# Kernel tuning notes

Measured on AMD Instinct MI355X. Metric: run time of the kernel, lower is better.

## Reference

```python
import jax, jax.numpy as jnp
import numpy as np

B, S, D, H = 16, 512, 1024, 16
DK = D // H
DFF = 4 * D
EPS = 1e-5
NEG = -1e9


def fake_quant(w):
    # EMA int8 symmetric per-tensor fake quantization of weights (inference view)
    scale = jnp.max(jnp.abs(w)) / 127.0
    wq = jnp.round(w / scale) * scale
    # straight-through estimator form (no-op in fwd)
    return w + jax.lax.stop_gradient(wq - w)


def layer_norm(x, g, b):
    mu = jnp.mean(x, axis=-1, keepdims=True)
    var = jnp.mean(jnp.square(x - mu), axis=-1, keepdims=True)
    return (x - mu) * jax.lax.rsqrt(var + EPS) * g + b


def setup_inputs() -> dict:
    key = jax.random.key(0)
    ks = jax.random.split(key, 16)
    std = 0.02
    inp = {
        'x': jax.random.normal(ks[0], (B, S, D), jnp.float32),
        'mask': jax.random.randint(ks[1], (B, 1, S, S), 0, 2, jnp.int32),
        'wq': jax.random.normal(ks[2], (D, D), jnp.float32) * std,
        'bq': jnp.zeros((D,), jnp.float32),
        'wk': jax.random.normal(ks[3], (D, D), jnp.float32) * std,
        'bk': jnp.zeros((D,), jnp.float32),
        'wv': jax.random.normal(ks[4], (D, D), jnp.float32) * std,
        'bv': jnp.zeros((D,), jnp.float32),
        'wo': jax.random.normal(ks[5], (D, D), jnp.float32) * std,
        'bo': jnp.zeros((D,), jnp.float32),
        'w1': jax.random.normal(ks[6], (D, DFF), jnp.float32) * std,
        'b1': jnp.zeros((DFF,), jnp.float32),
        'w2': jax.random.normal(ks[7], (DFF, D), jnp.float32) * std,
        'b2': jnp.zeros((D,), jnp.float32),
        'ln1_g': jnp.ones((D,), jnp.float32),
        'ln1_b': jnp.zeros((D,), jnp.float32),
        'ln2_g': jnp.ones((D,), jnp.float32),
        'ln2_b': jnp.zeros((D,), jnp.float32),
        'layer': 0,
    }
    return inp


def reference(x, mask, wq, bq, wk, bk, wv, bv, wo, bo, w1, b1, w2, b2,
              ln1_g, ln1_b, ln2_g, ln2_b, layer):
    # --- input sublayer: x + attention(LN(x)) (dropout = identity at eval) ---
    h = layer_norm(x, ln1_g, ln1_b)
    q = (h @ fake_quant(wq) + bq).reshape(B, S, H, DK).transpose(0, 2, 1, 3)
    k = (h @ fake_quant(wk) + bk).reshape(B, S, H, DK).transpose(0, 2, 1, 3)
    v = (h @ fake_quant(wv) + bv).reshape(B, S, H, DK).transpose(0, 2, 1, 3)
    scores = jnp.einsum('bhqd,bhkd->bhqk', q, k) * (1.0 / np.sqrt(DK))
    scores = jnp.where(mask == 0, NEG, scores)
    p = jax.nn.softmax(scores, axis=-1)
    attn = jnp.einsum('bhqk,bhkd->bhqd', p, v)
    attn = attn.transpose(0, 2, 1, 3).reshape(B, S, D)
    x = x + (attn @ wo + bo)
    # --- output sublayer: x + FFN(LN(x)), gelu (exact), middle_drop=False ---
    h2 = layer_norm(x, ln2_g, ln2_b)
    ff = jax.nn.gelu(h2 @ w1 + b1, approximate=False) @ w2 + b2
    return x + ff
```

## Files before the change

kernel.cpp:

```cpp
#include <hip/hip_runtime.h>
#include <hip/hip_bf16.h>
#include <math.h>

#define B_   16
#define S_   512
#define D_   1024
#define H_   16
#define DK_  64
#define DFF_ 4096
#define NROW (B_ * S_)
#define NEG_ (-1.0e9f)
#define SCQ_ 0.18033688011112042f

typedef __attribute__((ext_vector_type(8))) short short8v;
typedef __attribute__((ext_vector_type(4))) float f32x4;

__device__ __forceinline__ void load_lds16(const void* g, void* l) {
    __builtin_amdgcn_global_load_lds(
        reinterpret_cast<const __attribute__((address_space(1))) unsigned int*>(
            reinterpret_cast<uintptr_t>(g)),
        reinterpret_cast<__attribute__((address_space(3))) unsigned int*>(
            reinterpret_cast<uintptr_t>(l)),
        16, 0, 0);
}

__device__ __forceinline__ ushort f2bf_raw(float f) {
    __hip_bfloat16 h = __float2bfloat16(f);
    return *(ushort*)&h;
}

__device__ __forceinline__ float gelu_f(float v) {
    return 0.5f * v * (1.0f + erff(v * 0.70710678118654752f));
}

__global__ __launch_bounds__(256) void maskpack_k(
    const int* __restrict__ mask, unsigned long long* __restrict__ bits,
    unsigned int* __restrict__ scales) {
    if (blockIdx.x == 0 && threadIdx.x < 3) scales[threadIdx.x] = 0u;
    const int g = blockIdx.x * 4 + (threadIdx.x >> 6);
    const unsigned long long bm = __ballot(mask[(size_t)g * 64 + (threadIdx.x & 63)] != 0);
    if ((threadIdx.x & 63) == 0) bits[g] = bm;
}

__global__ __launch_bounds__(256) void maxabs3_k(
    const float* __restrict__ wq, const float* __restrict__ wk,
    const float* __restrict__ wv, unsigned int* __restrict__ out, int n) {
    const int wi = blockIdx.y;
    const float* w = wi == 0 ? wq : (wi == 1 ? wk : wv);
    float m = 0.f;
    for (int i = blockIdx.x * blockDim.x + threadIdx.x; i < n; i += gridDim.x * blockDim.x)
        m = fmaxf(m, fabsf(w[i]));
#pragma unroll
    for (int off = 1; off < 64; off <<= 1)
        m = fmaxf(m, __shfl_xor(m, off));
    __shared__ float red[4];
    const int wave = threadIdx.x >> 6;
    if ((threadIdx.x & 63) == 0) red[wave] = m;
    __syncthreads();
    if (threadIdx.x == 0) {
        m = fmaxf(fmaxf(red[0], red[1]), fmaxf(red[2], red[3]));
        atomicMax(out + wi, __float_as_uint(m));
    }
}

__global__ __launch_bounds__(256) void transq_all_k(
    const float* __restrict__ wq, const float* __restrict__ wk,
    const float* __restrict__ wv, const float* __restrict__ wo,
    const float* __restrict__ w1, const float* __restrict__ w2,
    const unsigned int* __restrict__ scales,
    __hip_bfloat16* __restrict__ wcat,
    __hip_bfloat16* __restrict__ wot,
    __hip_bfloat16* __restrict__ w1t, __hip_bfloat16* __restrict__ w2t)
{
    const int bid = blockIdx.x;
    int wi, rem, nbn, K, N;
    if (bid < 4096)      { wi = bid >> 10; rem = bid & 1023; nbn = 32;  K = 1024; N = 1024; }
    else if (bid < 8192) { wi = 4; rem = bid - 4096;         nbn = 128; K = 1024; N = 4096; }
    else                 { wi = 5; rem = bid - 8192;         nbn = 32;  K = 4096; N = 1024; }
    const float* W = wi == 0 ? wq : wi == 1 ? wk : wi == 2 ? wv : wi == 3 ? wo : wi == 4 ? w1 : w2;
    __hip_bfloat16* Wt = wi < 3 ? wcat + (size_t)wi * 1024 * 1024
                       : wi == 3 ? wot : wi == 4 ? w1t : w2t;
    const int n0 = (rem % nbn) * 32, k0 = (rem / nbn) * 32;

    __shared__ float t[32][33];
    const int tx = threadIdx.x, ty = threadIdx.y;
    float scale = 1.0f;
    const bool doq = wi < 3;
    if (doq) scale = __uint_as_float(scales[wi]) * (1.0f / 127.0f);
#pragma unroll
    for (int i = 0; i < 4; ++i) {
        float v = W[(size_t)(k0 + ty + 8 * i) * N + n0 + tx];
        if (doq) v = rintf(v / scale) * scale;
        t[ty + 8 * i][tx] = v;
    }
    __syncthreads();
#pragma unroll
    for (int i = 0; i < 4; ++i)
        Wt[(size_t)(n0 + ty + 8 * i) * K + k0 + tx] = __float2bfloat16(t[tx][ty + 8 * i]);
}

__global__ __launch_bounds__(256) void ln_bf16_k(
    const float* __restrict__ x, const float* __restrict__ g,
    const float* __restrict__ b, __hip_bfloat16* __restrict__ y)
{
    const int row = blockIdx.x;
    const int tid = threadIdx.x;
    const float4 v = *(const float4*)&x[(size_t)row * D_ + tid * 4];

    float s = v.x + v.y + v.z + v.w;
#pragma unroll
    for (int off = 1; off < 64; off <<= 1) s += __shfl_xor(s, off);
    __shared__ float red[8];
    const int wave = tid >> 6, lane = tid & 63;
    if (lane == 0) red[wave] = s;
    __syncthreads();
    s = red[0] + red[1] + red[2] + red[3];
    const float mu = s * (1.0f / (float)D_);

    const float d0 = v.x - mu, d1 = v.y - mu, d2 = v.z - mu, d3 = v.w - mu;
    float sq = d0 * d0 + d1 * d1 + d2 * d2 + d3 * d3;
#pragma unroll
    for (int off = 1; off < 64; off <<= 1) sq += __shfl_xor(sq, off);
    if (lane == 0) red[4 + wave] = sq;
    __syncthreads();
    sq = red[4] + red[5] + red[6] + red[7];
    const float rs = 1.0f / sqrtf(sq * (1.0f / (float)D_) + 1e-5f);

    const float4 gv = *(const float4*)&g[tid * 4];
    const float4 bv = *(const float4*)&b[tid * 4];
    union { ushort4 u4; ushort u[4]; } cv;
    cv.u[0] = f2bf_raw(d0 * rs * gv.x + bv.x);
    cv.u[1] = f2bf_raw(d1 * rs * gv.y + bv.y);
    cv.u[2] = f2bf_raw(d2 * rs * gv.z + bv.z);
    cv.u[3] = f2bf_raw(d3 * rs * gv.w + bv.w);
    *(ushort4*)&y[(size_t)row * D_ + tid * 4] = cv.u4;
}

template <int BNT, int EPI>
__global__ __launch_bounds__(512, 2) void gemm256(
    const __hip_bfloat16* __restrict__ A, const __hip_bfloat16* __restrict__ Bt,
    const float* __restrict__ bias, const float* __restrict__ bias2,
    const float* __restrict__ bias3, const float* __restrict__ res,
    void* __restrict__ C, void* __restrict__ C2, void* __restrict__ C3,
    int M, int N, int K)
{
    constexpr int BN   = BNT * 64;
    constexpr int ABYT = 256 * 128;
    constexpr int BBYT = BN * 128;
    constexpr int BUF  = ABYT + BBYT;
    constexpr int SB   = BNT / 2;
    __shared__ __align__(16) char smem[2 * BUF];

    const int tid = threadIdx.x;
    const int w = tid >> 6, lane = tid & 63;
    const int llo = lane & 15, lhi = lane >> 4;
    const int wr = w >> 2, wc = w & 3;

    const int nwg = gridDim.x;
    const int bid = blockIdx.x;
    const int swz = (bid & 7) * (nwg >> 3) + (bid >> 3);
    const int nby = M >> 8;
    const int by = swz % nby, bx = swz / nby;
    const int row0 = by * 256, col0 = bx * BN;

    const int cko0 = ((lhi) ^ (llo & 7)) * 16;
    const int cko1 = ((4 + lhi) ^ (llo & 7)) * 16;

    const int l3 = lane >> 3;
    const int klog8 = ((lane & 7) ^ l3) * 8;
    const int rA_base = ((w >> 1) & 3) * 16 + (w & 1) * 8 + l3;
    const int rB_ws = w * 8 + l3;

    const __hip_bfloat16* Asrc[2][2];
#pragma unroll
    for (int h = 0; h < 2; ++h)
#pragma unroll
        for (int s = 0; s < 2; ++s)
            Asrc[h][s] = A + (size_t)(row0 + s * 128 + h * 64 + rA_base) * K + klog8;
    const __hip_bfloat16* Bsrc[2][2];
#pragma unroll
    for (int h = 0; h < 2; ++h)
#pragma unroll
        for (int s = 0; s < 2; ++s)
            Bsrc[h][s] = Bt + (size_t)(col0 + h * (BN / 2) + (SB == 2 ? s * 64 : 0) + rB_ws) * K + klog8;

#define STAGE_A(bufv, hh, tt) do {                                                            \
    load_lds16(Asrc[hh][0] + (size_t)(tt) * 64, smem + (bufv) * BUF + (hh) * 16384 + w * 1024);        \
    load_lds16(Asrc[hh][1] + (size_t)(tt) * 64, smem + (bufv) * BUF + (hh) * 16384 + 8192 + w * 1024); \
} while (0)
#define STAGE_B(bufv, hh, tt) do {                                                                     \
    load_lds16(Bsrc[hh][0] + (size_t)(tt) * 64, smem + (bufv) * BUF + ABYT + (hh) * (BBYT / 2) + w * 1024); \
    if (SB == 2)                                                                                       \
        load_lds16(Bsrc[hh][1] + (size_t)(tt) * 64, smem + (bufv) * BUF + ABYT + (hh) * (BBYT / 2) + 8192 + w * 1024); \
} while (0)

    f32x4 acc[8][BNT] = {};
    const int NT = K >> 6;

    STAGE_B(0, 0, 0); STAGE_B(0, 1, 0); STAGE_A(0, 0, 0); STAGE_A(0, 1, 0);
    asm volatile("s_waitcnt vmcnt(0)");
    __builtin_amdgcn_s_barrier();

    short8v bfr[BNT][2];
    for (int t = 0; t < NT; ++t) {
        const int buf = t & 1;
        const bool more = (t + 1) < NT;
        char* const base = smem + buf * BUF;
#pragma unroll
        for (int ph = 0; ph < 4; ++ph) {
            if (ph == 0) {
#pragma unroll
                for (int n = 0; n < BNT; ++n) {
                    const int brow = wc * (BNT * 16) + n * 16 + llo;
                    bfr[n][0] = *(const short8v*)(base + ABYT + brow * 128 + cko0);
                    bfr[n][1] = *(const short8v*)(base + ABYT + brow * 128 + cko1);
                }
            }
            const int mf0 = ph * 2, mf1 = ph * 2 + 1;
            const int slot0 = (mf0 >> 2) * 128 + wr * 64 + (mf0 & 3) * 16 + llo;
            const int slot1 = (mf1 >> 2) * 128 + wr * 64 + (mf1 & 3) * 16 + llo;
            const short8v a0k0 = *(const short8v*)(base + slot0 * 128 + cko0);
            const short8v a0k1 = *(const short8v*)(base + slot0 * 128 + cko1);
            const short8v a1k0 = *(const short8v*)(base + slot1 * 128 + cko0);
            const short8v a1k1 = *(const short8v*)(base + slot1 * 128 + cko1);
            if (more) {
                if (ph == 0) { STAGE_B(buf ^ 1, 0, t + 1); STAGE_B(buf ^ 1, 1, t + 1); }
                else if (ph == 1) { STAGE_A(buf ^ 1, 0, t + 1); STAGE_A(buf ^ 1, 1, t + 1); }
            }
            __builtin_amdgcn_s_barrier();
            __builtin_amdgcn_s_setprio(1);
#pragma unroll
            for (int n = 0; n < BNT; ++n) {
                acc[mf0][n] = __builtin_amdgcn_mfma_f32_16x16x32_bf16(a0k0, bfr[n][0], acc[mf0][n], 0, 0, 0);
                acc[mf0][n] = __builtin_amdgcn_mfma_f32_16x16x32_bf16(a0k1, bfr[n][1], acc[mf0][n], 0, 0, 0);
                acc[mf1][n] = __builtin_amdgcn_mfma_f32_16x16x32_bf16(a1k0, bfr[n][0], acc[mf1][n], 0, 0, 0);
                acc[mf1][n] = __builtin_amdgcn_mfma_f32_16x16x32_bf16(a1k1, bfr[n][1], acc[mf1][n], 0, 0, 0);
            }
            __builtin_amdgcn_s_setprio(0);
            if (ph == 3) { asm volatile("s_waitcnt vmcnt(0)"); }
            __builtin_amdgcn_s_barrier();
        }
    }
#undef STAGE_A
#undef STAGE_B

    if (EPI == 3) {
#pragma unroll
        for (int n = 0; n < BNT; ++n) {
            const int col = col0 + wc * (BNT * 16) + n * 16 + llo;
            const int proj = col0 >> 10;
            const int lcol = col & 1023;
            const float bs = (proj == 0 ? bias : proj == 1 ? bias2 : bias3)[lcol];
#pragma unroll
            for (int mf = 0; mf < 8; ++mf) {
                const int rbase = row0 + wr * 128 + mf * 16 + lhi * 4;
                if (proj == 2) {
                    const int bb = rbase >> 9, srow = rbase & 511;
                    const int hh = lcol >> 6, dk = lcol & 63;
                    union { ushort4 u4; ushort u[4]; } pk;
#pragma unroll
                    for (int j = 0; j < 4; ++j) pk.u[j] = f2bf_raw(acc[mf][n][j] + bs);
                    *(ushort4*)&((ushort*)C3)[(((size_t)(bb * 16 + hh) * 64 + dk) << 9) + srow] = pk.u4;
                } else {
                    __hip_bfloat16* dst = proj == 0 ? (__hip_bfloat16*)C : (__hip_bfloat16*)C2;
                    const float sc = proj == 0 ? SCQ_ : 1.0f;
#pragma unroll
                    for (int j = 0; j < 4; ++j)
                        dst[(size_t)(rbase + j) * D_ + lcol] = __float2bfloat16((acc[mf][n][j] + bs) * sc);
                }
            }
        }
    } else {
        constexpr int WCOL = BNT * 16;
        constexpr int ESTR = WCOL + 4;
        float* const eslab = (float*)smem + w * (16 * ESTR);
        const int rr = lane >> 2;
        const int cq = lane & 3;
        const int c0 = cq * (BNT * 4);
        const int gcolb = col0 + wc * WCOL + c0;
#pragma unroll
        for (int mf = 0; mf < 8; ++mf) {
#pragma unroll
            for (int n = 0; n < BNT; ++n)
#pragma unroll
                for (int j = 0; j < 4; ++j)
                    eslab[(lhi * 4 + j) * ESTR + n * 16 + llo] = acc[mf][n][j];
            const int grow = row0 + wr * 128 + mf * 16 + rr;
            if (EPI == 1) {
                ushort tmp[BNT * 4];
#pragma unroll
                for (int i = 0; i < BNT; ++i) {
                    float4 v = *(float4*)&eslab[rr * ESTR + c0 + i * 4];
                    const float4 b4 = *(const float4*)&bias[gcolb + i * 4];
                    tmp[i * 4 + 0] = f2bf_raw(gelu_f(v.x + b4.x));
                    tmp[i * 4 + 1] = f2bf_raw(gelu_f(v.y + b4.y));
                    tmp[i * 4 + 2] = f2bf_raw(gelu_f(v.z + b4.z));
                    tmp[i * 4 + 3] = f2bf_raw(gelu_f(v.w + b4.w));
                }
                ushort* dst = (ushort*)C + (size_t)grow * N + gcolb;
#pragma unroll
                for (int i = 0; i < BNT / 2; ++i)
                    *(short8v*)(dst + i * 8) = *(short8v*)&tmp[i * 8];
            } else {
#pragma unroll
                for (int i = 0; i < BNT; ++i) {
                    float4 v = *(float4*)&eslab[rr * ESTR + c0 + i * 4];
                    const float4 b4 = *(const float4*)&bias[gcolb + i * 4];
                    const float4 r4 = *(const float4*)&res[(size_t)grow * N + gcolb + i * 4];
                    v.x += b4.x + r4.x;
                    v.y += b4.y + r4.y;
                    v.z += b4.z + r4.z;
                    v.w += b4.w + r4.w;
                    *(float4*)&((float*)C)[(size_t)grow * N + gcolb + i * 4] = v;
                }
            }
        }
    }
}

__global__ __launch_bounds__(256) void attn_mfma_k(
    const __hip_bfloat16* __restrict__ q, const __hip_bfloat16* __restrict__ k,
    const __hip_bfloat16* __restrict__ vt, const unsigned long long* __restrict__ mbits,
    __hip_bfloat16* __restrict__ o)
{
    const int qt = blockIdx.x;
    const int bh = blockIdx.y;
    const int b = bh >> 4, h = bh & 15;

    __shared__ __align__(16) __hip_bfloat16 Qs[64 * 72];
    __shared__ __align__(16) __hip_bfloat16 Ks[64 * 72];
    __shared__ __align__(16) __hip_bfloat16 Vts[64 * 72];
    __shared__ __align__(16) __hip_bfloat16 Pt[64 * 72];

    const int tid = threadIdx.x;
    const int w = tid >> 6, l = tid & 63;
    const int llo = l & 15, lhi = l >> 4;
    const int srow = tid >> 2, schk = tid & 3;

    {
        const __hip_bfloat16* qg =
            q + (size_t)(b * S_ + qt * 64 + srow) * D_ + h * 64 + schk * 16;
        *(short8v*)&Qs[srow * 72 + schk * 16] = *(const short8v*)qg;
        *(short8v*)&Qs[srow * 72 + schk * 16 + 8] = *(const short8v*)(qg + 8);
    }

    const __hip_bfloat16* kptr = k + (size_t)(b * S_ + srow) * D_ + h * 64 + schk * 16;
    const __hip_bfloat16* vptr = vt + (((size_t)(b * 16 + h) * 64 + srow) << 9) + schk * 16;
    short8v kr0 = *(const short8v*)kptr;
    short8v kr1 = *(const short8v*)(kptr + 8);
    short8v vr0 = *(const short8v*)vptr;
    short8v vr1 = *(const short8v*)(vptr + 8);

    __syncthreads();

    const short8v qa0 = *(const short8v*)&Qs[(w * 16 + llo) * 72 + lhi * 8];
    const short8v qa1 = *(const short8v*)&Qs[(w * 16 + llo) * 72 + 32 + lhi * 8];

    const unsigned long long* mrow =
        mbits + (((size_t)(b * S_ + qt * 64 + w * 16 + lhi * 4)) << 3);

    f32x4 oacc[4] = {};
    float m_r[4] = {-INFINITY, -INFINITY, -INFINITY, -INFINITY};
    float l_r[4] = {0.f, 0.f, 0.f, 0.f};

    for (int kt = 0; kt < 8; ++kt) {
        *(short8v*)&Ks[srow * 72 + schk * 16] = kr0;
        *(short8v*)&Ks[srow * 72 + schk * 16 + 8] = kr1;
        *(short8v*)&Vts[srow * 72 + schk * 16] = vr0;
        *(short8v*)&Vts[srow * 72 + schk * 16 + 8] = vr1;
        __syncthreads();

        short8v nk0, nk1, nv0, nv1;
        if (kt < 7) {
            const __hip_bfloat16* kp = kptr + (size_t)(kt + 1) * (64 * D_);
            const __hip_bfloat16* vp = vptr + (kt + 1) * 64;
            nk0 = *(const short8v*)kp;
            nk1 = *(const short8v*)(kp + 8);
            nv0 = *(const short8v*)vp;
            nv1 = *(const short8v*)(vp + 8);
        }

        f32x4 sacc[4] = {};
#pragma unroll
        for (int n = 0; n < 4; ++n)
            sacc[n] = __builtin_amdgcn_mfma_f32_16x16x32_bf16(
                qa0, *(const short8v*)&Ks[(n * 16 + llo) * 72 + lhi * 8], sacc[n], 0, 0, 0);
#pragma unroll
        for (int n = 0; n < 4; ++n)
            sacc[n] = __builtin_amdgcn_mfma_f32_16x16x32_bf16(
                qa1, *(const short8v*)&Ks[(n * 16 + llo) * 72 + 32 + lhi * 8], sacc[n], 0, 0, 0);

#pragma unroll
        for (int j = 0; j < 4; ++j) {
            const unsigned long long mb = mrow[j * 8 + kt];
            const float s0 = ((mb >> llo) & 1ull)        ? sacc[0][j] : NEG_;
            const float s1 = ((mb >> (llo + 16)) & 1ull) ? sacc[1][j] : NEG_;
            const float s2 = ((mb >> (llo + 32)) & 1ull) ? sacc[2][j] : NEG_;
            const float s3 = ((mb >> (llo + 48)) & 1ull) ? sacc[3][j] : NEG_;
            float pm = fmaxf(fmaxf(s0, s1), fmaxf(s2, s3));
            pm = fmaxf(pm, __shfl_xor(pm, 1));
            pm = fmaxf(pm, __shfl_xor(pm, 2));
            pm = fmaxf(pm, __shfl_xor(pm, 4));
            pm = fmaxf(pm, __shfl_xor(pm, 8));
            float alpha = 1.0f;
            if (!__all(pm <= m_r[j] + 8.0f)) {
                const float mnew = fmaxf(m_r[j], pm);
                alpha = exp2f(m_r[j] - mnew);
                m_r[j] = mnew;
#pragma unroll
                for (int df = 0; df < 4; ++df) oacc[df][j] *= alpha;
            }
            const float p0 = exp2f(s0 - m_r[j]);
            const float p1 = exp2f(s1 - m_r[j]);
            const float p2 = exp2f(s2 - m_r[j]);
            const float p3 = exp2f(s3 - m_r[j]);
            float rsum = p0 + p1 + p2 + p3;
            rsum += __shfl_xor(rsum, 1);
            rsum += __shfl_xor(rsum, 2);
            rsum += __shfl_xor(rsum, 4);
            rsum += __shfl_xor(rsum, 8);
            l_r[j] = l_r[j] * alpha + rsum;
            const int prow = (w * 16 + lhi * 4 + j) * 72;
            Pt[prow + llo]      = __float2bfloat16(p0);
            Pt[prow + llo + 16] = __float2bfloat16(p1);
            Pt[prow + llo + 32] = __float2bfloat16(p2);
            Pt[prow + llo + 48] = __float2bfloat16(p3);
        }

#pragma unroll
        for (int ks = 0; ks < 2; ++ks) {
            const short8v pa = *(const short8v*)&Pt[(w * 16 + llo) * 72 + ks * 32 + lhi * 8];
#pragma unroll
            for (int df = 0; df < 4; ++df) {
                const short8v vb = *(const short8v*)&Vts[(df * 16 + llo) * 72 + ks * 32 + lhi * 8];
                oacc[df] = __builtin_amdgcn_mfma_f32_16x16x32_bf16(pa, vb, oacc[df], 0, 0, 0);
            }
        }
        __syncthreads();

        if (kt < 7) { kr0 = nk0; kr1 = nk1; vr0 = nv0; vr1 = nv1; }
    }

#pragma unroll
    for (int j = 0; j < 4; ++j) {
        const float inv = 1.0f / l_r[j];
        __hip_bfloat16* orow =
            o + (size_t)(b * S_ + qt * 64 + w * 16 + lhi * 4 + j) * D_ + h * 64;
#pragma unroll
        for (int df = 0; df < 4; ++df)
            orow[df * 16 + llo] = __float2bfloat16(oacc[df][j] * inv);
    }
}

extern "C" void kernel_launch(void* const* d_in, const int* in_sizes, int n_in,
                              void* d_out, int out_size, void* d_ws, size_t ws_size,
                              hipStream_t stream)
{
    const float* x    = (const float*)d_in[0];
    const int*   mask = (const int*)d_in[1];
    const float* wq   = (const float*)d_in[2];
    const float* bq   = (const float*)d_in[3];
    const float* wk   = (const float*)d_in[4];
    const float* bk   = (const float*)d_in[5];
    const float* wv   = (const float*)d_in[6];
    const float* bv   = (const float*)d_in[7];
    const float* wo   = (const float*)d_in[8];
    const float* bo   = (const float*)d_in[9];
    const float* w1   = (const float*)d_in[10];
    const float* b1   = (const float*)d_in[11];
    const float* w2   = (const float*)d_in[12];
    const float* b2   = (const float*)d_in[13];
    const float* ln1g = (const float*)d_in[14];
    const float* ln1b = (const float*)d_in[15];
    const float* ln2g = (const float*)d_in[16];
    const float* ln2b = (const float*)d_in[17];
    float* out = (float*)d_out;
    char* ws = (char*)d_ws;

    const size_t MB = 1024 * 1024;
    __hip_bfloat16* hb    = (__hip_bfloat16*)(ws);
    __hip_bfloat16* qbh   = (__hip_bfloat16*)(ws + 16 * MB);
    __hip_bfloat16* kbh   = (__hip_bfloat16*)(ws + 32 * MB);
    __hip_bfloat16* vth   = (__hip_bfloat16*)(ws + 48 * MB);
    __hip_bfloat16* attnb = (__hip_bfloat16*)(ws + 64 * MB);
    __hip_bfloat16* ff1b  = (__hip_bfloat16*)(ws + 16 * MB);
    __hip_bfloat16* wcat  = (__hip_bfloat16*)(ws + 80 * MB);
    __hip_bfloat16* wot   = (__hip_bfloat16*)(ws + 86 * MB);
    __hip_bfloat16* w1t   = (__hip_bfloat16*)(ws + 88 * MB);
    __hip_bfloat16* w2t   = (__hip_bfloat16*)(ws + 96 * MB);
    unsigned int*   scales = (unsigned int*)(ws + 104 * MB);
    unsigned long long* mbits = (unsigned long long*)(ws + 105 * MB);

    maskpack_k<<<(B_ * S_ * (S_ / 64)) / 4, 256, 0, stream>>>(mask, mbits, scales);
    maxabs3_k<<<dim3(256, 3), 256, 0, stream>>>(wq, wk, wv, scales, D_ * D_);
    transq_all_k<<<12288, dim3(32, 8), 0, stream>>>(
        wq, wk, wv, wo, w1, w2, scales, wcat, wot, w1t, w2t);

    ln_bf16_k<<<NROW, 256, 0, stream>>>(x, ln1g, ln1b, hb);

    gemm256<4, 3><<<(3 * D_ / 256) * (NROW / 256), 512, 0, stream>>>(
        hb, wcat, bq, bk, bv, nullptr, qbh, kbh, vth, NROW, 3 * D_, D_);

    attn_mfma_k<<<dim3(S_ / 64, B_ * H_), 256, 0, stream>>>(qbh, kbh, vth, mbits, attnb);

    gemm256<2, 2><<<(D_ / 128) * (NROW / 256), 512, 0, stream>>>(
        attnb, wot, bo, nullptr, nullptr, x, out, nullptr, nullptr, NROW, D_, D_);

    ln_bf16_k<<<NROW, 256, 0, stream>>>(out, ln2g, ln2b, hb);

    gemm256<4, 1><<<(DFF_ / 256) * (NROW / 256), 512, 0, stream>>>(
        hb, w1t, b1, nullptr, nullptr, nullptr, ff1b, nullptr, nullptr, NROW, DFF_, D_);

    gemm256<2, 2><<<(D_ / 128) * (NROW / 256), 512, 0, stream>>>(
        ff1b, w2t, b2, nullptr, nullptr, out, out, nullptr, nullptr, NROW, D_, DFF_);
}
```

Baseline: 420.3 us.

## Replace 256-row GEMM tiles with 128x128 tiles on 4-wave workgroups

Replaces the 512-thread GEMM kernel, which used 256-row tiles with 256- or 128-column variants, by a single 256-thread kernel with 128x128 tiles and a 2x2 wave layout. Each wave now owns a 64x64 output block. The aim is more workgroups and higher occupancy, with lower register pressure from the smaller accumulator set. In exchange the MFMA-to-LDS-load ratio drops and operands are reloaded more often, so global and LDS traffic per FLOP goes up.

```diff
diff --git a/kernel.cpp b/kernel.cpp
--- a/kernel.cpp
+++ b/kernel.cpp
@@ -136,72 +136,65 @@
     *(ushort4*)&y[(size_t)row * D_ + tid * 4] = cv.u4;
 }
 
-template <int BNT, int EPI>
-__global__ __launch_bounds__(512, 2) void gemm256(
+template <int EPI>
+__global__ __launch_bounds__(256, 2) void gemm128d(
     const __hip_bfloat16* __restrict__ A, const __hip_bfloat16* __restrict__ Bt,
     const float* __restrict__ bias, const float* __restrict__ bias2,
     const float* __restrict__ bias3, const float* __restrict__ res,
     void* __restrict__ C, void* __restrict__ C2, void* __restrict__ C3,
     int M, int N, int K)
 {
-    constexpr int BN   = BNT * 64;
-    constexpr int ABYT = 256 * 128;
-    constexpr int BBYT = BN * 128;
-    constexpr int BUF  = ABYT + BBYT;
-    constexpr int SB   = BNT / 2;
+    constexpr int ABYT = 128 * 128;
+    constexpr int BUF  = 2 * ABYT;
     __shared__ __align__(16) char smem[2 * BUF];
 
     const int tid = threadIdx.x;
     const int w = tid >> 6, lane = tid & 63;
     const int llo = lane & 15, lhi = lane >> 4;
-    const int wr = w >> 2, wc = w & 3;
-
-    const int nwg = gridDim.x;
-    const int bid = blockIdx.x;
+    const int wr = w >> 1, wc = w & 1;
+
+    const int nwg = gridDim.x, bid = blockIdx.x;
     const int swz = (bid & 7) * (nwg >> 3) + (bid >> 3);
-    const int nby = M >> 8;
+    const int nby = M >> 7;
     const int by = swz % nby, bx = swz / nby;
-    const int row0 = by * 256, col0 = bx * BN;
+    const int row0 = by * 128, col0 = bx * 128;
 
     const int cko0 = ((lhi) ^ (llo & 7)) * 16;
     const int cko1 = ((4 + lhi) ^ (llo & 7)) * 16;
 
     const int l3 = lane >> 3;
     const int klog8 = ((lane & 7) ^ l3) * 8;
-    const int rA_base = ((w >> 1) & 3) * 16 + (w & 1) * 8 + l3;
-    const int rB_ws = w * 8 + l3;
-
-    const __hip_bfloat16* Asrc[2][2];
-#pragma unroll
-    for (int h = 0; h < 2; ++h)
-#pragma unroll
-        for (int s = 0; s < 2; ++s)
-            Asrc[h][s] = A + (size_t)(row0 + s * 128 + h * 64 + rA_base) * K + klog8;
-    const __hip_bfloat16* Bsrc[2][2];
-#pragma unroll
-    for (int h = 0; h < 2; ++h)
-#pragma unroll
-        for (int s = 0; s < 2; ++s)
-            Bsrc[h][s] = Bt + (size_t)(col0 + h * (BN / 2) + (SB == 2 ? s * 64 : 0) + rB_ws) * K + klog8;
-
-#define STAGE_A(bufv, hh, tt) do {                                                            \
-    load_lds16(Asrc[hh][0] + (size_t)(tt) * 64, smem + (bufv) * BUF + (hh) * 16384 + w * 1024);        \
-    load_lds16(Asrc[hh][1] + (size_t)(tt) * 64, smem + (bufv) * BUF + (hh) * 16384 + 8192 + w * 1024); \
+    const int rws = w * 8 + l3;
+
+    const __hip_bfloat16* Asrc[4];
+    const __hip_bfloat16* Bsrc[4];
+#pragma unroll
+    for (int q = 0; q < 4; ++q) {
+        Asrc[q] = A + (size_t)(row0 + q * 32 + rws) * K + klog8;
+        Bsrc[q] = Bt + (size_t)(col0 + q * 32 + rws) * K + klog8;
+    }
+
+#define STAGE_A4(bufv, tt) do {                                                   \
+    load_lds16(Asrc[0] + (size_t)(tt) * 64, smem + (bufv) * BUF + 0 * 4096 + w * 1024); \
+    load_lds16(Asrc[1] + (size_t)(tt) * 64, smem + (bufv) * BUF + 1 * 4096 + w * 1024); \
+    load_lds16(Asrc[2] + (size_t)(tt) * 64, smem + (bufv) * BUF + 2 * 4096 + w * 1024); \
+    load_lds16(Asrc[3] + (size_t)(tt) * 64, smem + (bufv) * BUF + 3 * 4096 + w * 1024); \
 } while (0)
-#define STAGE_B(bufv, hh, tt) do {                                                                     \
-    load_lds16(Bsrc[hh][0] + (size_t)(tt) * 64, smem + (bufv) * BUF + ABYT + (hh) * (BBYT / 2) + w * 1024); \
-    if (SB == 2)                                                                                       \
-        load_lds16(Bsrc[hh][1] + (size_t)(tt) * 64, smem + (bufv) * BUF + ABYT + (hh) * (BBYT / 2) + 8192 + w * 1024); \
+#define STAGE_B4(bufv, tt) do {                                                          \
+    load_lds16(Bsrc[0] + (size_t)(tt) * 64, smem + (bufv) * BUF + ABYT + 0 * 4096 + w * 1024); \
+    load_lds16(Bsrc[1] + (size_t)(tt) * 64, smem + (bufv) * BUF + ABYT + 1 * 4096 + w * 1024); \
+    load_lds16(Bsrc[2] + (size_t)(tt) * 64, smem + (bufv) * BUF + ABYT + 2 * 4096 + w * 1024); \
+    load_lds16(Bsrc[3] + (size_t)(tt) * 64, smem + (bufv) * BUF + ABYT + 3 * 4096 + w * 1024); \
 } while (0)
 
-    f32x4 acc[8][BNT] = {};
+    f32x4 acc[4][4] = {};
     const int NT = K >> 6;
 
-    STAGE_B(0, 0, 0); STAGE_B(0, 1, 0); STAGE_A(0, 0, 0); STAGE_A(0, 1, 0);
+    STAGE_B4(0, 0); STAGE_A4(0, 0);
     asm volatile("s_waitcnt vmcnt(0)");
     __builtin_amdgcn_s_barrier();
 
-    short8v bfr[BNT][2];
+    short8v bfr[4][2];
     for (int t = 0; t < NT; ++t) {
         const int buf = t & 1;
         const bool more = (t + 1) < NT;
@@ -210,50 +203,44 @@
         for (int ph = 0; ph < 4; ++ph) {
             if (ph == 0) {
 #pragma unroll
-                for (int n = 0; n < BNT; ++n) {
-                    const int brow = wc * (BNT * 16) + n * 16 + llo;
+                for (int n = 0; n < 4; ++n) {
+                    const int brow = wc * 64 + n * 16 + llo;
                     bfr[n][0] = *(const short8v*)(base + ABYT + brow * 128 + cko0);
                     bfr[n][1] = *(const short8v*)(base + ABYT + brow * 128 + cko1);
                 }
             }
-            const int mf0 = ph * 2, mf1 = ph * 2 + 1;
-            const int slot0 = (mf0 >> 2) * 128 + wr * 64 + (mf0 & 3) * 16 + llo;
-            const int slot1 = (mf1 >> 2) * 128 + wr * 64 + (mf1 & 3) * 16 + llo;
-            const short8v a0k0 = *(const short8v*)(base + slot0 * 128 + cko0);
-            const short8v a0k1 = *(const short8v*)(base + slot0 * 128 + cko1);
-            const short8v a1k0 = *(const short8v*)(base + slot1 * 128 + cko0);
-            const short8v a1k1 = *(const short8v*)(base + slot1 * 128 + cko1);
+            const int slot = wr * 64 + ph * 16 + llo;
+            const short8v ak0 = *(const short8v*)(base + slot * 128 + cko0);
+            const short8v ak1 = *(const short8v*)(base + slot * 128 + cko1);
             if (more) {
-                if (ph == 0) { STAGE_B(buf ^ 1, 0, t + 1); STAGE_B(buf ^ 1, 1, t + 1); }
-                else if (ph == 1) { STAGE_A(buf ^ 1, 0, t + 1); STAGE_A(buf ^ 1, 1, t + 1); }
+                if (ph == 0) STAGE_B4(buf ^ 1, t + 1);
+                else if (ph == 1) STAGE_A4(buf ^ 1, t + 1);
             }
             __builtin_amdgcn_s_barrier();
             __builtin_amdgcn_s_setprio(1);
 #pragma unroll
-            for (int n = 0; n < BNT; ++n) {
-                acc[mf0][n] = __builtin_amdgcn_mfma_f32_16x16x32_bf16(a0k0, bfr[n][0], acc[mf0][n], 0, 0, 0);
-                acc[mf0][n] = __builtin_amdgcn_mfma_f32_16x16x32_bf16(a0k1, bfr[n][1], acc[mf0][n], 0, 0, 0);
-                acc[mf1][n] = __builtin_amdgcn_mfma_f32_16x16x32_bf16(a1k0, bfr[n][0], acc[mf1][n], 0, 0, 0);
-                acc[mf1][n] = __builtin_amdgcn_mfma_f32_16x16x32_bf16(a1k1, bfr[n][1], acc[mf1][n], 0, 0, 0);
+            for (int n = 0; n < 4; ++n) {
+                acc[ph][n] = __builtin_amdgcn_mfma_f32_16x16x32_bf16(ak0, bfr[n][0], acc[ph][n], 0, 0, 0);
+                acc[ph][n] = __builtin_amdgcn_mfma_f32_16x16x32_bf16(ak1, bfr[n][1], acc[ph][n], 0, 0, 0);
             }
             __builtin_amdgcn_s_setprio(0);
             if (ph == 3) { asm volatile("s_waitcnt vmcnt(0)"); }
             __builtin_amdgcn_s_barrier();
         }
     }
-#undef STAGE_A
-#undef STAGE_B
+#undef STAGE_A4
+#undef STAGE_B4
 
     if (EPI == 3) {
 #pragma unroll
-        for (int n = 0; n < BNT; ++n) {
-            const int col = col0 + wc * (BNT * 16) + n * 16 + llo;
+        for (int n = 0; n < 4; ++n) {
+            const int col = col0 + wc * 64 + n * 16 + llo;
             const int proj = col0 >> 10;
             const int lcol = col & 1023;
             const float bs = (proj == 0 ? bias : proj == 1 ? bias2 : bias3)[lcol];
 #pragma unroll
-            for (int mf = 0; mf < 8; ++mf) {
-                const int rbase = row0 + wr * 128 + mf * 16 + lhi * 4;
+            for (int mf = 0; mf < 4; ++mf) {
+                const int rbase = row0 + wr * 64 + mf * 16 + lhi * 4;
                 if (proj == 2) {
                     const int bb = rbase >> 9, srow = rbase & 511;
                     const int hh = lcol >> 6, dk = lcol & 63;
@@ -271,25 +258,23 @@
             }
         }
     } else {
-        constexpr int WCOL = BNT * 16;
-        constexpr int ESTR = WCOL + 4;
+        constexpr int ESTR = 68;
         float* const eslab = (float*)smem + w * (16 * ESTR);
         const int rr = lane >> 2;
-        const int cq = lane & 3;
-        const int c0 = cq * (BNT * 4);
-        const int gcolb = col0 + wc * WCOL + c0;
-#pragma unroll
-        for (int mf = 0; mf < 8; ++mf) {
-#pragma unroll
-            for (int n = 0; n < BNT; ++n)
+        const int c0 = (lane & 3) * 16;
+        const int gcolb = col0 + wc * 64 + c0;
+#pragma unroll
+        for (int mf = 0; mf < 4; ++mf) {
+#pragma unroll
+            for (int n = 0; n < 4; ++n)
 #pragma unroll
                 for (int j = 0; j < 4; ++j)
                     eslab[(lhi * 4 + j) * ESTR + n * 16 + llo] = acc[mf][n][j];
-            const int grow = row0 + wr * 128 + mf * 16 + rr;
+            const int grow = row0 + wr * 64 + mf * 16 + rr;
             if (EPI == 1) {
-                ushort tmp[BNT * 4];
-#pragma unroll
-                for (int i = 0; i < BNT; ++i) {
+                ushort tmp[16];
+#pragma unroll
+                for (int i = 0; i < 4; ++i) {
                     float4 v = *(float4*)&eslab[rr * ESTR + c0 + i * 4];
                     const float4 b4 = *(const float4*)&bias[gcolb + i * 4];
                     tmp[i * 4 + 0] = f2bf_raw(gelu_f(v.x + b4.x));
@@ -298,12 +283,11 @@
                     tmp[i * 4 + 3] = f2bf_raw(gelu_f(v.w + b4.w));
                 }
                 ushort* dst = (ushort*)C + (size_t)grow * N + gcolb;
-#pragma unroll
-                for (int i = 0; i < BNT / 2; ++i)
-                    *(short8v*)(dst + i * 8) = *(short8v*)&tmp[i * 8];
+                *(short8v*)(dst) = *(short8v*)&tmp[0];
+                *(short8v*)(dst + 8) = *(short8v*)&tmp[8];
             } else {
 #pragma unroll
-                for (int i = 0; i < BNT; ++i) {
+                for (int i = 0; i < 4; ++i) {
                     float4 v = *(float4*)&eslab[rr * ESTR + c0 + i * 4];
                     const float4 b4 = *(const float4*)&bias[gcolb + i * 4];
                     const float4 r4 = *(const float4*)&res[(size_t)grow * N + gcolb + i * 4];
@@ -498,19 +482,19 @@
 
     ln_bf16_k<<<NROW, 256, 0, stream>>>(x, ln1g, ln1b, hb);
 
-    gemm256<4, 3><<<(3 * D_ / 256) * (NROW / 256), 512, 0, stream>>>(
+    gemm128d<3><<<(3 * D_ / 128) * (NROW / 128), 256, 0, stream>>>(
         hb, wcat, bq, bk, bv, nullptr, qbh, kbh, vth, NROW, 3 * D_, D_);
 
     attn_mfma_k<<<dim3(S_ / 64, B_ * H_), 256, 0, stream>>>(qbh, kbh, vth, mbits, attnb);
 
-    gemm256<2, 2><<<(D_ / 128) * (NROW / 256), 512, 0, stream>>>(
+    gemm128d<2><<<(D_ / 128) * (NROW / 128), 256, 0, stream>>>(
         attnb, wot, bo, nullptr, nullptr, x, out, nullptr, nullptr, NROW, D_, D_);
 
     ln_bf16_k<<<NROW, 256, 0, stream>>>(out, ln2g, ln2b, hb);
 
-    gemm256<4, 1><<<(DFF_ / 256) * (NROW / 256), 512, 0, stream>>>(
+    gemm128d<1><<<(DFF_ / 128) * (NROW / 128), 256, 0, stream>>>(
         hb, w1t, b1, nullptr, nullptr, nullptr, ff1b, nullptr, nullptr, NROW, DFF_, D_);
 
-    gemm256<2, 2><<<(D_ / 128) * (NROW / 256), 512, 0, stream>>>(
+    gemm128d<2><<<(D_ / 128) * (NROW / 128), 256, 0, stream>>>(
         ff1b, w2t, b2, nullptr, nullptr, out, out, nullptr, nullptr, NROW, D_, DFF_);
 }
```

Result: slower. 435.7 us (+3.7%).
